# Performance work log

Measured on AMD Instinct MI355X. Metric: run time of the kernel, lower is better.

The kernel has to match this reference:

```python
import jax, jax.numpy as jnp
import numpy as np

HEADS = 4  # from init_kwargs

def _branch_index(seq_len: int) -> jnp.ndarray:
    # position 0 -> layer_s(0), 1 -> layer_r(1), 2 -> layer_o(2),
    # then alternating layer_a(3)/layer_v(4) starting at position 3.
    tail = jnp.where((jnp.arange(seq_len - 3) % 2) == 0, 3, 4)
    return jnp.concatenate([jnp.array([0, 1, 2], dtype=tail.dtype), tail])


def setup_inputs() -> dict:
    key = jax.random.key(0)
    k1, k2, k3 = jax.random.split(key, 3)
    B, S, H = 128, 513, 256
    x = jax.random.normal(k1, (B, S, H), dtype=jnp.float32)
    # 5 Linear layers, nn.Linear convention: y = x @ W.T + b, W: [out,in]
    W = jax.random.normal(k2, (5, H, H), dtype=jnp.float32) * (1.0 / np.sqrt(H))
    b = jax.random.normal(k3, (5, H), dtype=jnp.float32) * 0.02
    return {"x": x, "W": W, "b": b}


def reference(x, W, b):
    # Original applies each Linear to a position-masked copy of x and sums.
    # Since the 5 masks are disjoint one-hots over positions, the weight term
    # at position t is x[t] @ W[m(t)].T; the bias term is sum of ALL 5 biases
    # (Linear(0) = bias), applied at every position.
    B, S, H = x.shape
    idx = _branch_index(S)            # [S] in {0..4}
    Wsel = W[idx]
    out = jnp.einsum('bsh,sdh->bsd', x, Wsel) + b.sum(axis=0)
    return out.reshape(B, S, HEADS, H // HEADS)
```

## Files before the change

kernel.cpp:

```cpp
#include <hip/hip_runtime.h>
#include <hip/hip_bf16.h>

#define B_ 128
#define S_ 513
#define H_ 256
#define SH_ (S_ * H_)

typedef __attribute__((ext_vector_type(8))) short short8;
typedef __attribute__((ext_vector_type(4))) float f32x4;

static __device__ inline short8 pack8(float4 a, float4 b) {
    union { short8 s; __hip_bfloat162 h[4]; } u;
    u.h[0] = __float22bfloat162_rn(make_float2(a.x, a.y));
    u.h[1] = __float22bfloat162_rn(make_float2(a.z, a.w));
    u.h[2] = __float22bfloat162_rn(make_float2(b.x, b.y));
    u.h[3] = __float22bfloat162_rn(make_float2(b.z, b.w));
    return u.s;
}

__global__ void prep_kernel(const float* __restrict__ W,
                            const float* __restrict__ bias,
                            unsigned short* __restrict__ Wbf,
                            float* __restrict__ bsum) {
    int t = blockIdx.x * 256 + threadIdx.x;
    if (t < 5 * 32 * 256) {
        int m  = t >> 13;
        int r  = t & 8191;
        int d  = r >> 5;
        int kc = r & 31;
        const float* src = W + (((size_t)m * 256 + d) * 256 + kc * 8);
        float4 v0 = *(const float4*)src;
        float4 v1 = *(const float4*)(src + 4);
        *(short8*)(Wbf + ((size_t)(m * 32 + kc) * 256 + d) * 8) = pack8(v0, v1);
    }
    if (t < H_) {
        float s = 0.f;
#pragma unroll
        for (int i = 0; i < 5; ++i) s += bias[i * H_ + t];
        bsum[t] = s;
    }
}

template <int MODE>
__global__ __launch_bounds__(256, 4)
void sel_gemm_kernel(const float* __restrict__ x,
                     const void* __restrict__ Wp,
                     const void* __restrict__ bp,
                     float* __restrict__ out) {
    const int bid = blockIdx.x;
    int m_idx, rmax, rowstride;
    size_t rowbase;
    if (bid < 1024) {
        const int b    = bid >> 3;
        const int sub  = bid & 7;
        const int par  = sub & 1;
        const int tile = sub >> 1;
        const int sbase = (par ? 3 : 4) + tile * 128;
        m_idx     = par ? 3 : 4;
        rowbase   = (size_t)b * S_ + sbase;
        rowstride = 2;
        rmax      = (512 - sbase) >> 1;
        if (rmax > 63) rmax = 63;
    } else {
        const int e  = bid - 1024;
        const int s  = e >> 1;
        const int bh = e & 1;
        m_idx     = s;
        rowbase   = (size_t)bh * 64 * S_ + s;
        rowstride = S_;
        rmax      = 63;
    }

    __shared__ unsigned short As[64 * 256];

    const int t    = threadIdx.x;
    const int lane = t & 63;
    const int w    = t >> 6;
    const int lrow = lane & 15;
    const int quad = lane >> 4;

#pragma unroll
    for (int i = 0; i < 8; ++i) {
        int flat = i * 256 + t;
        int r = flat >> 5;
        int c = flat & 31;
        int rc = r <= rmax ? r : rmax;
        const float* src = x + (rowbase + (size_t)rowstride * rc) * H_ + c * 8;
        float4 v0 = *(const float4*)src;
        float4 v1 = *(const float4*)(src + 4);
        *(short8*)&As[r * 256 + ((c ^ (r & 7)) * 8)] = pack8(v0, v1);
    }

    f32x4 acc[4][4];
#pragma unroll
    for (int i = 0; i < 4; ++i)
#pragma unroll
        for (int j = 0; j < 4; ++j) {
            f32x4 z = {0.f, 0.f, 0.f, 0.f};
            acc[i][j] = z;
        }

    __syncthreads();

#pragma unroll
    for (int kk = 0; kk < 8; ++kk) {
        short8 wfr[4];
        if (MODE == 0) {
            const unsigned short* Wk =
                (const unsigned short*)Wp +
                ((size_t)(m_idx * 32 + kk * 4 + quad) * 256) * 8;
#pragma unroll
            for (int j = 0; j < 4; ++j)
                wfr[j] = *(const short8*)(Wk + (size_t)(w * 64 + j * 16 + lrow) * 8);
        } else {
            const float* Wb = (const float*)Wp + (size_t)m_idx * H_ * H_;
#pragma unroll
            for (int j = 0; j < 4; ++j) {
                const float* wrow = Wb + (size_t)(w * 64 + j * 16 + lrow) * H_
                                    + kk * 32 + quad * 8;
                float4 v0 = *(const float4*)wrow;
                float4 v1 = *(const float4*)(wrow + 4);
                wfr[j] = pack8(v0, v1);
            }
        }

        short8 xfr[4];
        const int cc = kk * 4 + quad;
#pragma unroll
        for (int i = 0; i < 4; ++i) {
            int r = i * 16 + lrow;
            xfr[i] = *(const short8*)&As[r * 256 + ((cc ^ (r & 7)) * 8)];
        }

#pragma unroll
        for (int j = 0; j < 4; ++j)
#pragma unroll
            for (int i = 0; i < 4; ++i)
                acc[i][j] = __builtin_amdgcn_mfma_f32_16x16x32_bf16(
                    wfr[j], xfr[i], acc[i][j], 0, 0, 0);
    }

#pragma unroll
    for (int j = 0; j < 4; ++j) {
        const int d0 = w * 64 + j * 16 + quad * 4;
        f32x4 bj;
        if (MODE == 0) {
            bj = *(const f32x4*)((const float*)bp + d0);
        } else {
            const float* bias = (const float*)bp;
#pragma unroll
            for (int r = 0; r < 4; ++r) {
                float sum = 0.f;
#pragma unroll
                for (int i = 0; i < 5; ++i) sum += bias[i * H_ + d0 + r];
                bj[r] = sum;
            }
        }
#pragma unroll
        for (int i = 0; i < 4; ++i) {
            const int r = i * 16 + lrow;
            if (r <= rmax) {
                f32x4 v = acc[i][j] + bj;
                *(f32x4*)(out + (rowbase + (size_t)rowstride * r) * H_ + d0) = v;
            }
        }
    }
}

extern "C" void kernel_launch(void* const* d_in, const int* in_sizes, int n_in,
                              void* d_out, int out_size, void* d_ws, size_t ws_size,
                              hipStream_t stream) {
    const float* x    = (const float*)d_in[0];
    const float* W    = (const float*)d_in[1];
    const float* bias = (const float*)d_in[2];
    float* out = (float*)d_out;

    const size_t w_elems  = (size_t)5 * H_ * H_;
    const size_t ws_need  = w_elems * sizeof(unsigned short) + H_ * sizeof(float);

    const int grid = 1024 + 6;
    if (ws_size >= ws_need) {
        unsigned short* Wbf = (unsigned short*)d_ws;
        float* bsum = (float*)((char*)d_ws + w_elems * sizeof(unsigned short));
        prep_kernel<<<dim3(160), dim3(256), 0, stream>>>(W, bias, Wbf, bsum);
        sel_gemm_kernel<0><<<dim3(grid), dim3(256), 0, stream>>>(
            x, (const void*)Wbf, (const void*)bsum, out);
    } else {
        sel_gemm_kernel<1><<<dim3(grid), dim3(256), 0, stream>>>(
            x, (const void*)W, (const void*)bias, out);
    }
}
```

Measured before the change: 128.7 us.

## Load x tiles directly into LDS as fp32 and halve row tiles

The x tile is now staged with direct global-to-LDS loads, using an XOR swizzle on the source address. It stays fp32 in LDS and is converted to bf16 when the MFMA fragments are read, instead of passing through registers and being converted during staging. Each block now covers 32 rows instead of 64, which doubles the grid to give more blocks in flight to hide memory latency on this bandwidth-bound selective GEMM. In exchange, weight fragments are re-read twice as often across blocks, and each MFMA fragment read needs extra conversion work.

```diff
diff --git a/kernel.cpp b/kernel.cpp
--- a/kernel.cpp
+++ b/kernel.cpp
@@ -15,6 +15,14 @@
     u.h[1] = __float22bfloat162_rn(make_float2(a.z, a.w));
     u.h[2] = __float22bfloat162_rn(make_float2(b.x, b.y));
     u.h[3] = __float22bfloat162_rn(make_float2(b.z, b.w));
+    return u.s;
+}
+static __device__ inline short8 pack8v(f32x4 a, f32x4 b) {
+    union { short8 s; __hip_bfloat162 h[4]; } u;
+    u.h[0] = __float22bfloat162_rn(make_float2(a[0], a[1]));
+    u.h[1] = __float22bfloat162_rn(make_float2(a[2], a[3]));
+    u.h[2] = __float22bfloat162_rn(make_float2(b[0], b[1]));
+    u.h[3] = __float22bfloat162_rn(make_float2(b[2], b[3]));
     return u.s;
 }
 
@@ -50,28 +58,28 @@
     const int bid = blockIdx.x;
     int m_idx, rmax, rowstride;
     size_t rowbase;
-    if (bid < 1024) {
-        const int b    = bid >> 3;
-        const int sub  = bid & 7;
+    if (bid < 2048) {
+        const int b    = bid >> 4;
+        const int sub  = bid & 15;
         const int par  = sub & 1;
         const int tile = sub >> 1;
-        const int sbase = (par ? 3 : 4) + tile * 128;
+        const int sbase = (par ? 3 : 4) + tile * 64;
         m_idx     = par ? 3 : 4;
         rowbase   = (size_t)b * S_ + sbase;
         rowstride = 2;
         rmax      = (512 - sbase) >> 1;
-        if (rmax > 63) rmax = 63;
+        if (rmax > 31) rmax = 31;
     } else {
-        const int e  = bid - 1024;
-        const int s  = e >> 1;
-        const int bh = e & 1;
+        const int e  = bid - 2048;
+        const int s  = e >> 2;
+        const int bq = e & 3;
         m_idx     = s;
-        rowbase   = (size_t)bh * 64 * S_ + s;
+        rowbase   = (size_t)(bq * 32) * S_ + s;
         rowstride = S_;
-        rmax      = 63;
-    }
-
-    __shared__ unsigned short As[64 * 256];
+        rmax      = 31;
+    }
+
+    __shared__ float As[32 * 256];
 
     const int t    = threadIdx.x;
     const int lane = t & 63;
@@ -80,20 +88,20 @@
     const int quad = lane >> 4;
 
 #pragma unroll
-    for (int i = 0; i < 8; ++i) {
-        int flat = i * 256 + t;
-        int r = flat >> 5;
-        int c = flat & 31;
-        int rc = r <= rmax ? r : rmax;
-        const float* src = x + (rowbase + (size_t)rowstride * rc) * H_ + c * 8;
-        float4 v0 = *(const float4*)src;
-        float4 v1 = *(const float4*)(src + 4);
-        *(short8*)&As[r * 256 + ((c ^ (r & 7)) * 8)] = pack8(v0, v1);
-    }
-
-    f32x4 acc[4][4];
-#pragma unroll
-    for (int i = 0; i < 4; ++i)
+    for (int it = 0; it < 8; ++it) {
+        const int r  = it * 4 + w;
+        const int rc = r <= rmax ? r : rmax;
+        const float* src = x + (rowbase + (size_t)rowstride * rc) * H_
+                             + ((lane ^ (r & 7)) << 2);
+        __builtin_amdgcn_global_load_lds(
+            (const __attribute__((address_space(1))) unsigned int*)src,
+            (__attribute__((address_space(3))) unsigned int*)&As[r * 256],
+            16, 0, 0);
+    }
+
+    f32x4 acc[2][4];
+#pragma unroll
+    for (int i = 0; i < 2; ++i)
 #pragma unroll
         for (int j = 0; j < 4; ++j) {
             f32x4 z = {0.f, 0.f, 0.f, 0.f};
@@ -124,18 +132,20 @@
             }
         }
 
-        short8 xfr[4];
-        const int cc = kk * 4 + quad;
-#pragma unroll
-        for (int i = 0; i < 4; ++i) {
-            int r = i * 16 + lrow;
-            xfr[i] = *(const short8*)&As[r * 256 + ((cc ^ (r & 7)) * 8)];
+        short8 xfr[2];
+        const int g0 = kk * 8 + quad * 2;
+#pragma unroll
+        for (int i = 0; i < 2; ++i) {
+            const int r = i * 16 + lrow;
+            f32x4 f0 = *(const f32x4*)&As[r * 256 + (((g0    ) ^ (r & 7)) << 2)];
+            f32x4 f1 = *(const f32x4*)&As[r * 256 + (((g0 + 1) ^ (r & 7)) << 2)];
+            xfr[i] = pack8v(f0, f1);
         }
 
 #pragma unroll
         for (int j = 0; j < 4; ++j)
 #pragma unroll
-            for (int i = 0; i < 4; ++i)
+            for (int i = 0; i < 2; ++i)
                 acc[i][j] = __builtin_amdgcn_mfma_f32_16x16x32_bf16(
                     wfr[j], xfr[i], acc[i][j], 0, 0, 0);
     }
@@ -157,7 +167,7 @@
             }
         }
 #pragma unroll
-        for (int i = 0; i < 4; ++i) {
+        for (int i = 0; i < 2; ++i) {
             const int r = i * 16 + lrow;
             if (r <= rmax) {
                 f32x4 v = acc[i][j] + bj;
@@ -178,7 +188,7 @@
     const size_t w_elems  = (size_t)5 * H_ * H_;
     const size_t ws_need  = w_elems * sizeof(unsigned short) + H_ * sizeof(float);
 
-    const int grid = 1024 + 6;
+    const int grid = 2048 + 12;
     if (ws_size >= ws_need) {
         unsigned short* Wbf = (unsigned short*)d_ws;
         float* bsum = (float*)((char*)d_ws + w_elems * sizeof(unsigned short));
```

Measured after the change: 132.0 us. +2.5%, slower.
